# Kernel optimization log

Measured on AMD Instinct MI355X. Metric: run time of the kernel, lower is better.

Reference implementation:

```python
import jax, jax.numpy as jnp
import numpy as np

NUM_CLUSTERS = 512
TEMPERATURE = 1.0
MAX_ITERS = 10
EPSILON = 1e-4
N, D = 65536, 256


def setup_inputs() -> dict:
    key = jax.random.key(0)
    weights = jax.random.normal(key, (N, D), dtype=jnp.float32)
    return {"weights": weights}


def _neg_dist(w, c):
    # -||w_i - c_j||_2 computed via the expanded quadratic form to avoid
    # materializing the [N, K, D] broadcast tensor the torch code builds.
    d2 = (jnp.sum(w * w, axis=1, keepdims=True)
          - 2.0 * (w @ c.T)
          + jnp.sum(c * c, axis=1)[None, :])
    return -jnp.sqrt(jnp.maximum(d2, 1e-12))  # [N, K]


def reference(weights):
    # deterministic stand-in for torch.randperm init: first K rows
    clusters0 = weights[:NUM_CLUSTERS]                                 # [K, D]
    attn0 = jnp.zeros((weights.shape[0], NUM_CLUSTERS), weights.dtype)  # [N, K]
    done0 = jnp.array(False)

    def step(carry, _):
        clusters, attn, done = carry
        attn_new = jax.nn.softmax(_neg_dist(weights, clusters) / TEMPERATURE, axis=-1)
        weighted_sum = attn_new.T @ weights            # [K, D]
        counts = attn_new.sum(axis=0)                  # [K]
        new_clusters = weighted_sum / counts[:, None]
        small = jnp.linalg.norm(clusters - new_clusters) <= EPSILON
        # torch loop: attn is computed BEFORE the break check, clusters only
        # advance if not converged; once done everything is frozen.
        attn_out = jnp.where(done, attn, attn_new)
        clusters_out = jnp.where(done | small, clusters, new_clusters)
        return (clusters_out, attn_out, done | small), None

    (clusters, attn, _), _ = jax.lax.scan(step, (clusters0, attn0, done0), None, length=MAX_ITERS)
    compressed_weights = attn @ clusters               # [N, D]
    return compressed_weights, clusters, attn
```

## Files before the change

kernel.cpp:

```cpp
#include <hip/hip_runtime.h>
#include <math.h>

#define NPTS  65536
#define DIM   256
#define NC    512
#define NITER 10

#define WS_C      0
#define WS_WSUM   (WS_C + NC*DIM)
#define WS_COUNTS (WS_WSUM + NC*DIM)
#define WS_W2     (WS_COUNTS + NC)
#define WS_C2     (WS_W2 + NPTS)
#define WS_DONE   (WS_C2 + NC)
#define WS_CHI    (WS_DONE + 4)
#define WS_CLO    (WS_CHI + NC*DIM/2)

typedef __attribute__((ext_vector_type(8))) short bf16x8;
typedef __attribute__((ext_vector_type(4))) float f32x4;

__device__ __forceinline__ unsigned short f2bf(float x) {
  unsigned u = __float_as_uint(x);
  u += 0x7fffu + ((u >> 16) & 1u);
  return (unsigned short)(u >> 16);
}
__device__ __forceinline__ float bf2f(unsigned short h) {
  return __uint_as_float(((unsigned)h) << 16);
}

__global__ void k_init(const float* __restrict__ W, float* __restrict__ C, int* __restrict__ done) {
  int i = blockIdx.x * 256 + threadIdx.x;
  C[i] = W[i];
  if (i == 0) *done = 0;
}

__global__ void k_w2(const float* __restrict__ W, float* __restrict__ w2) {
  int row  = blockIdx.x * 4 + (threadIdx.x >> 6);
  int lane = threadIdx.x & 63;
  float4 v = *(const float4*)(W + (size_t)row * DIM + 4 * lane);
  float s = v.x*v.x + v.y*v.y + v.z*v.z + v.w*v.w;
  #pragma unroll
  for (int o = 32; o; o >>= 1) s += __shfl_down(s, o);
  if (lane == 0) w2[row] = s;
}

__global__ void k_prep(const float* __restrict__ C, float* __restrict__ c2,
                       float* __restrict__ wsum, float* __restrict__ counts,
                       unsigned short* __restrict__ Chi, unsigned short* __restrict__ Clo) {
  __shared__ float wsh[4];
  int b = blockIdx.x, t = threadIdx.x;
  float v = C[b * DIM + t];
  unsigned short h = f2bf(v);
  Chi[b * DIM + t] = h;
  Clo[b * DIM + t] = f2bf(v - bf2f(h));
  float s = v * v;
  #pragma unroll
  for (int o = 32; o; o >>= 1) s += __shfl_down(s, o);
  if ((t & 63) == 0) wsh[t >> 6] = s;
  __syncthreads();
  if (t == 0) c2[b] = wsh[0] + wsh[1] + wsh[2] + wsh[3];
  wsum[b * DIM + t] = 0.f;
  if (t == 0) counts[b] = 0.f;
}

__launch_bounds__(256, 4)
__global__ void k_attn(const float* __restrict__ W,
                       const unsigned short* __restrict__ Chi,
                       const unsigned short* __restrict__ Clo,
                       const float* __restrict__ w2, const float* __restrict__ c2,
                       float* __restrict__ attn, float* __restrict__ counts,
                       const int* __restrict__ done)
{
  if (*done) return;
  __shared__ unsigned short Bh[2][4096];
  __shared__ unsigned short Bl[2][4096];
  __shared__ float c2s[NC];
  __shared__ float rinv_sh[64];
  __shared__ float cnt_lds[NC];

  const int t    = threadIdx.x;
  const int wave = t >> 6;
  const int lane = t & 63;
  const int lx   = lane & 15;
  const int gy   = lane >> 4;
  const int rowW = blockIdx.x * 64 + wave * 16;

  cnt_lds[t] = 0.f; cnt_lds[t + 256] = 0.f;
  c2s[t] = c2[t];   c2s[t + 256] = c2[t + 256];

  bf16x8 ah[8], al[8];
  {
    const float* wrow = W + (size_t)(rowW + lx) * DIM;
    #pragma unroll
    for (int kc = 0; kc < 8; ++kc) {
      const float* p = wrow + kc * 32 + gy * 8;
      float4 v0 = *(const float4*)p;
      float4 v1 = *(const float4*)(p + 4);
      float xs[8] = {v0.x, v0.y, v0.z, v0.w, v1.x, v1.y, v1.z, v1.w};
      #pragma unroll
      for (int j = 0; j < 8; ++j) {
        unsigned short h = f2bf(xs[j]);
        ah[kc][j] = (short)h;
        al[kc][j] = (short)f2bf(xs[j] - bf2f(h));
      }
    }
  }
  float w2r[4];
  #pragma unroll
  for (int r = 0; r < 4; ++r) w2r[r] = w2[rowW + gy * 4 + r];

  float rowP[4] = {0.f, 0.f, 0.f, 0.f};
  float4 sh[2], sl[2];

  #define STAGE_LOAD(ct_)                                              \
    { _Pragma("unroll")                                                \
      for (int p = 0; p < 2; ++p) {                                    \
        int L = p * 256 + t;                                           \
        int kc = L >> 6, r = (L >> 2) & 15, g = L & 3;                 \
        int off = ((ct_) * 16 + r) * 256 + kc * 32 + g * 8;            \
        sh[p] = *(const float4*)(Chi + off);                           \
        sl[p] = *(const float4*)(Clo + off);                           \
      } }
  #define STAGE_WRITE(b_)                                              \
    { _Pragma("unroll")                                                \
      for (int p = 0; p < 2; ++p) {                                    \
        int L = p * 256 + t;                                           \
        *(float4*)&Bh[b_][L * 8] = sh[p];                              \
        *(float4*)&Bl[b_][L * 8] = sl[p];                              \
      } }

  STAGE_LOAD(0)
  STAGE_WRITE(0)
  __syncthreads();

  for (int ct = 0; ct < 32; ++ct) {
    const int cur = ct & 1;
    if (ct < 31) STAGE_LOAD(ct + 1)

    f32x4 aHH = {0.f,0.f,0.f,0.f}, aLH = {0.f,0.f,0.f,0.f}, aHL = {0.f,0.f,0.f,0.f};
    #pragma unroll
    for (int kc = 0; kc < 8; ++kc) {
      bf16x8 bh = *(const bf16x8*)&Bh[cur][kc * 512 + lx * 32 + gy * 8];
      bf16x8 bl = *(const bf16x8*)&Bl[cur][kc * 512 + lx * 32 + gy * 8];
      aHH = __builtin_amdgcn_mfma_f32_16x16x32_bf16(ah[kc], bh, aHH, 0, 0, 0);
      aLH = __builtin_amdgcn_mfma_f32_16x16x32_bf16(al[kc], bh, aLH, 0, 0, 0);
      aHL = __builtin_amdgcn_mfma_f32_16x16x32_bf16(ah[kc], bl, aHL, 0, 0, 0);
    }
    float c2v = c2s[ct * 16 + lx];
    #pragma unroll
    for (int r = 0; r < 4; ++r) {
      float dot = aHH[r] + aLH[r] + aHL[r];
      float d2  = w2r[r] + c2v - 2.f * dot;
      float e   = __expf(-sqrtf(fmaxf(d2, 1e-12f)));
      rowP[r] += e;
      attn[(size_t)(rowW + gy * 4 + r) * NC + ct * 16 + lx] = e;
    }
    __syncthreads();
    if (ct < 31) { STAGE_WRITE(cur ^ 1) __syncthreads(); }
  }

  #pragma unroll
  for (int m = 1; m < 16; m <<= 1) {
    #pragma unroll
    for (int r = 0; r < 4; ++r) rowP[r] += __shfl_xor(rowP[r], m);
  }
  if (lx == 0) {
    #pragma unroll
    for (int r = 0; r < 4; ++r) rinv_sh[wave * 16 + gy * 4 + r] = 1.f / rowP[r];
  }
  __syncthreads();

  {
    float cs0 = 0.f, cs1 = 0.f, cs2 = 0.f, cs3 = 0.f;
    const int c0 = (t * 4) & 511;
    const size_t base = (size_t)blockIdx.x * 64 * NC;
    #pragma unroll 4
    for (int p = 0; p < 32; ++p) {
      int idx = p * 1024 + t * 4;
      int row = idx >> 9;
      float rv = rinv_sh[row];
      float* g = attn + base + (size_t)row * NC + c0;
      float4 v = *(float4*)g;
      v.x *= rv; v.y *= rv; v.z *= rv; v.w *= rv;
      *(float4*)g = v;
      cs0 += v.x; cs1 += v.y; cs2 += v.z; cs3 += v.w;
    }
    atomicAdd(&cnt_lds[c0 + 0], cs0);
    atomicAdd(&cnt_lds[c0 + 1], cs1);
    atomicAdd(&cnt_lds[c0 + 2], cs2);
    atomicAdd(&cnt_lds[c0 + 3], cs3);
  }
  __syncthreads();
  atomicAdd(&counts[t],       cnt_lds[t]);
  atomicAdd(&counts[t + 256], cnt_lds[t + 256]);
}

__launch_bounds__(256, 2)
__global__ void k_wsum(const float* __restrict__ attn, const float* __restrict__ W,
                       float* __restrict__ wsum, const int* __restrict__ done)
{
  if (*done) return;
  __shared__ float At[64*64];
  __shared__ float Bt[64*64];
  const int t = threadIdx.x, tx = t & 15, ty = t >> 4;
  const int ctile = blockIdx.x & 7;
  const int dtile = (blockIdx.x >> 3) & 3;
  const int kch   = blockIdx.x >> 5;
  const int c0 = ctile*64, d0 = dtile*64;
  const size_t rbase = (size_t)kch * 2048;
  float acc[4][4] = {{0}};
  for (int kk = 0; kk < 2048; kk += 64) {
    __syncthreads();
    #pragma unroll
    for (int p = 0; p < 4; ++p) {
      int q = p*256 + t;
      int kr = q >> 4, c4 = q & 15;
      size_t row = rbase + kk + kr;
      *(float4*)&At[kr*64 + 4*c4] = *(const float4*)(attn + row*NC  + c0 + 4*c4);
      *(float4*)&Bt[kr*64 + 4*c4] = *(const float4*)(W    + row*DIM + d0 + 4*c4);
    }
    __syncthreads();
    #pragma unroll 8
    for (int k = 0; k < 64; ++k) {
      float4 av = *(const float4*)&At[k*64 + 4*ty];
      float4 bv = *(const float4*)&Bt[k*64 + 4*tx];
      acc[0][0]+=av.x*bv.x; acc[0][1]+=av.x*bv.y; acc[0][2]+=av.x*bv.z; acc[0][3]+=av.x*bv.w;
      acc[1][0]+=av.y*bv.x; acc[1][1]+=av.y*bv.y; acc[1][2]+=av.y*bv.z; acc[1][3]+=av.y*bv.w;
      acc[2][0]+=av.z*bv.x; acc[2][1]+=av.z*bv.y; acc[2][2]+=av.z*bv.z; acc[2][3]+=av.z*bv.w;
      acc[3][0]+=av.w*bv.x; acc[3][1]+=av.w*bv.y; acc[3][2]+=av.w*bv.z; acc[3][3]+=av.w*bv.w;
    }
  }
  #pragma unroll
  for (int i = 0; i < 4; ++i)
    #pragma unroll
    for (int j = 0; j < 4; ++j)
      atomicAdd(&wsum[(size_t)(c0 + 4*ty + i)*DIM + d0 + 4*tx + j], acc[i][j]);
}

__global__ void k_update(float* __restrict__ C, const float* __restrict__ wsum,
                         const float* __restrict__ counts, int* __restrict__ done)
{
  if (*done) return;
  __shared__ float wsh[16];
  __shared__ float nrm2;
  int t = threadIdx.x;
  float local = 0.f;
  for (int p = 0; p < 128; ++p) {
    int i = p*1024 + t;
    float cn = wsum[i] / counts[i >> 8];
    float d  = C[i] - cn;
    local += d * d;
  }
  #pragma unroll
  for (int o = 32; o; o >>= 1) local += __shfl_down(local, o);
  if ((t & 63) == 0) wsh[t >> 6] = local;
  __syncthreads();
  if (t == 0) {
    float s = 0.f;
    #pragma unroll
    for (int x = 0; x < 16; ++x) s += wsh[x];
    nrm2 = s;
  }
  __syncthreads();
  if (nrm2 <= 1e-8f) {
    if (t == 0) *done = 1;
  } else {
    for (int p = 0; p < 128; ++p) {
      int i = p*1024 + t;
      C[i] = wsum[i] / counts[i >> 8];
    }
  }
}

__device__ __forceinline__ int swz64(int k, int c) {
  return (k << 6) + (c ^ (((k >> 2) & 15) << 2));
}
__launch_bounds__(256, 2)
__global__ void k_compress(const float* __restrict__ attn, const float* __restrict__ C,
                           float* __restrict__ out)
{
  __shared__ float At[64*64];
  __shared__ float Bt[64*64];
  const int t = threadIdx.x, tx = t & 15, ty = t >> 4;
  const int rt = blockIdx.x >> 2;
  const int dt = blockIdx.x & 3;
  const int r0 = rt*64, d0 = dt*64;
  float acc[4][4] = {{0}};
  for (int kc = 0; kc < 8; ++kc) {
    __syncthreads();
    #pragma unroll
    for (int p = 0; p < 4; ++p) {
      int q = p*256 + t;
      int r = q >> 4, x4 = q & 15;
      float4 v = *(const float4*)(attn + (size_t)(r0 + r)*NC + kc*64 + 4*x4);
      At[swz64(4*x4+0, r)] = v.x;
      At[swz64(4*x4+1, r)] = v.y;
      At[swz64(4*x4+2, r)] = v.z;
      At[swz64(4*x4+3, r)] = v.w;
      *(float4*)&Bt[r*64 + 4*x4] = *(const float4*)(C + (size_t)(kc*64 + r)*DIM + d0 + 4*x4);
    }
    __syncthreads();
    #pragma unroll 8
    for (int k = 0; k < 64; ++k) {
      float4 av = *(const float4*)&At[swz64(k, 4*ty)];
      float4 bv = *(const float4*)&Bt[k*64 + 4*tx];
      acc[0][0]+=av.x*bv.x; acc[0][1]+=av.x*bv.y; acc[0][2]+=av.x*bv.z; acc[0][3]+=av.x*bv.w;
      acc[1][0]+=av.y*bv.x; acc[1][1]+=av.y*bv.y; acc[1][2]+=av.y*bv.z; acc[1][3]+=av.y*bv.w;
      acc[2][0]+=av.z*bv.x; acc[2][1]+=av.z*bv.y; acc[2][2]+=av.z*bv.z; acc[2][3]+=av.z*bv.w;
      acc[3][0]+=av.w*bv.x; acc[3][1]+=av.w*bv.y; acc[3][2]+=av.w*bv.z; acc[3][3]+=av.w*bv.w;
    }
  }
  #pragma unroll
  for (int i = 0; i < 4; ++i) {
    float4 o = {acc[i][0], acc[i][1], acc[i][2], acc[i][3]};
    *(float4*)(out + (size_t)(r0 + 4*ty + i)*DIM + d0 + 4*tx) = o;
  }
}

__global__ void k_copy(const float* __restrict__ C, float* __restrict__ out) {
  int i = blockIdx.x * 256 + threadIdx.x;
  out[i] = C[i];
}

extern "C" void kernel_launch(void* const* d_in, const int* in_sizes, int n_in,
                              void* d_out, int out_size, void* d_ws, size_t ws_size,
                              hipStream_t stream)
{
  const float* W = (const float*)d_in[0];
  float* out = (float*)d_out;
  float* compressed   = out;
  float* out_clusters = out + (size_t)NPTS * DIM;
  float* attn         = out_clusters + NC * DIM;

  float* ws     = (float*)d_ws;
  float* C      = ws + WS_C;
  float* wsum   = ws + WS_WSUM;
  float* counts = ws + WS_COUNTS;
  float* w2     = ws + WS_W2;
  float* c2     = ws + WS_C2;
  int*   done   = (int*)(ws + WS_DONE);
  unsigned short* Chi = (unsigned short*)(ws + WS_CHI);
  unsigned short* Clo = (unsigned short*)(ws + WS_CLO);

  k_init<<<NC*DIM/256, 256, 0, stream>>>(W, C, done);
  k_w2<<<NPTS/4, 256, 0, stream>>>(W, w2);
  for (int it = 0; it < NITER; ++it) {
    k_prep<<<NC, 256, 0, stream>>>(C, c2, wsum, counts, Chi, Clo);
    k_attn<<<NPTS/64, 256, 0, stream>>>(W, Chi, Clo, w2, c2, attn, counts, done);
    k_wsum<<<1024, 256, 0, stream>>>(attn, W, wsum, done);
    k_update<<<1, 1024, 0, stream>>>(C, wsum, counts, done);
  }
  k_compress<<<(NPTS/64)*(DIM/64), 256, 0, stream>>>(attn, C, compressed);
  k_copy<<<NC*DIM/256, 256, 0, stream>>>(C, out_clusters);
}
```

Before: 4.360 ms.

## Defer softmax normalization into wsum and parallelize the cluster update

k_attn now writes unnormalized exponentials and stores per-row reciprocal sums in a global buffer. This removes the per-iteration read-modify-write pass over the 128MB attention matrix. k_wsum scales attention rows by rinv as it loads them and accumulates the cluster counts itself, and a single k_norm pass normalizes attn once at the end. Attention stores are staged through LDS so they go out as coalesced float4 writes, and the B tile becomes single-buffered. The single-block k_update is split into two grid-wide kernels, with the norm reduced through an atomic. The cost is extra kernel launches and more complex convergence bookkeeping.

```diff
diff --git a/kernel.cpp b/kernel.cpp
--- a/kernel.cpp
+++ b/kernel.cpp
@@ -8,11 +8,14 @@
 
 #define WS_C      0
 #define WS_WSUM   (WS_C + NC*DIM)
-#define WS_COUNTS (WS_WSUM + NC*DIM)
+#define WS_CNEW   (WS_WSUM + NC*DIM)
+#define WS_COUNTS (WS_CNEW + NC*DIM)
 #define WS_W2     (WS_COUNTS + NC)
 #define WS_C2     (WS_W2 + NPTS)
-#define WS_DONE   (WS_C2 + NC)
-#define WS_CHI    (WS_DONE + 4)
+#define WS_RINV   (WS_C2 + NC)
+#define WS_DONE   (WS_RINV + NPTS)
+#define WS_NRM    (WS_DONE + 1)
+#define WS_CHI    (WS_DONE + 7)
 #define WS_CLO    (WS_CHI + NC*DIM/2)
 
 typedef __attribute__((ext_vector_type(8))) short bf16x8;
@@ -45,7 +48,8 @@
 
 __global__ void k_prep(const float* __restrict__ C, float* __restrict__ c2,
                        float* __restrict__ wsum, float* __restrict__ counts,
-                       unsigned short* __restrict__ Chi, unsigned short* __restrict__ Clo) {
+                       unsigned short* __restrict__ Chi, unsigned short* __restrict__ Clo,
+                       float* __restrict__ nrm2) {
   __shared__ float wsh[4];
   int b = blockIdx.x, t = threadIdx.x;
   float v = C[b * DIM + t];
@@ -60,6 +64,7 @@
   if (t == 0) c2[b] = wsh[0] + wsh[1] + wsh[2] + wsh[3];
   wsum[b * DIM + t] = 0.f;
   if (t == 0) counts[b] = 0.f;
+  if (b == 0 && t == 0) *nrm2 = 0.f;
 }
 
 __launch_bounds__(256, 4)
@@ -67,15 +72,14 @@
                        const unsigned short* __restrict__ Chi,
                        const unsigned short* __restrict__ Clo,
                        const float* __restrict__ w2, const float* __restrict__ c2,
-                       float* __restrict__ attn, float* __restrict__ counts,
+                       float* __restrict__ attn, float* __restrict__ rinv,
                        const int* __restrict__ done)
 {
   if (*done) return;
-  __shared__ unsigned short Bh[2][4096];
-  __shared__ unsigned short Bl[2][4096];
+  __shared__ unsigned short Bh[4096];
+  __shared__ unsigned short Bl[4096];
   __shared__ float c2s[NC];
-  __shared__ float rinv_sh[64];
-  __shared__ float cnt_lds[NC];
+  __shared__ float ebuf[4][16][36];
 
   const int t    = threadIdx.x;
   const int wave = t >> 6;
@@ -84,8 +88,7 @@
   const int gy   = lane >> 4;
   const int rowW = blockIdx.x * 64 + wave * 16;
 
-  cnt_lds[t] = 0.f; cnt_lds[t + 256] = 0.f;
-  c2s[t] = c2[t];   c2s[t + 256] = c2[t + 256];
+  c2s[t] = c2[t];  c2s[t + 256] = c2[t + 256];
 
   bf16x8 ah[8], al[8];
   {
@@ -111,36 +114,38 @@
   float rowP[4] = {0.f, 0.f, 0.f, 0.f};
   float4 sh[2], sl[2];
 
-  #define STAGE_LOAD(ct_)                                              \
-    { _Pragma("unroll")                                                \
-      for (int p = 0; p < 2; ++p) {                                    \
-        int L = p * 256 + t;                                           \
-        int kc = L >> 6, r = (L >> 2) & 15, g = L & 3;                 \
-        int off = ((ct_) * 16 + r) * 256 + kc * 32 + g * 8;            \
-        sh[p] = *(const float4*)(Chi + off);                           \
-        sl[p] = *(const float4*)(Clo + off);                           \
-      } }
-  #define STAGE_WRITE(b_)                                              \
-    { _Pragma("unroll")                                                \
-      for (int p = 0; p < 2; ++p) {                                    \
-        int L = p * 256 + t;                                           \
-        *(float4*)&Bh[b_][L * 8] = sh[p];                              \
-        *(float4*)&Bl[b_][L * 8] = sl[p];                              \
-      } }
-
-  STAGE_LOAD(0)
-  STAGE_WRITE(0)
+  #pragma unroll
+  for (int p = 0; p < 2; ++p) {
+    int L = p * 256 + t;
+    int kc = L >> 6, r = (L >> 2) & 15, g = L & 3;
+    int off = r * 256 + kc * 32 + g * 8;
+    sh[p] = *(const float4*)(Chi + off);
+    sl[p] = *(const float4*)(Clo + off);
+  }
+  #pragma unroll
+  for (int p = 0; p < 2; ++p) {
+    int L = p * 256 + t;
+    *(float4*)&Bh[L * 8] = sh[p];
+    *(float4*)&Bl[L * 8] = sl[p];
+  }
   __syncthreads();
 
   for (int ct = 0; ct < 32; ++ct) {
-    const int cur = ct & 1;
-    if (ct < 31) STAGE_LOAD(ct + 1)
-
+    if (ct < 31) {
+      #pragma unroll
+      for (int p = 0; p < 2; ++p) {
+        int L = p * 256 + t;
+        int kc = L >> 6, r = (L >> 2) & 15, g = L & 3;
+        int off = ((ct + 1) * 16 + r) * 256 + kc * 32 + g * 8;
+        sh[p] = *(const float4*)(Chi + off);
+        sl[p] = *(const float4*)(Clo + off);
+      }
+    }
     f32x4 aHH = {0.f,0.f,0.f,0.f}, aLH = {0.f,0.f,0.f,0.f}, aHL = {0.f,0.f,0.f,0.f};
     #pragma unroll
     for (int kc = 0; kc < 8; ++kc) {
-      bf16x8 bh = *(const bf16x8*)&Bh[cur][kc * 512 + lx * 32 + gy * 8];
-      bf16x8 bl = *(const bf16x8*)&Bl[cur][kc * 512 + lx * 32 + gy * 8];
+      bf16x8 bh = *(const bf16x8*)&Bh[kc * 512 + lx * 32 + gy * 8];
+      bf16x8 bl = *(const bf16x8*)&Bl[kc * 512 + lx * 32 + gy * 8];
       aHH = __builtin_amdgcn_mfma_f32_16x16x32_bf16(ah[kc], bh, aHH, 0, 0, 0);
       aLH = __builtin_amdgcn_mfma_f32_16x16x32_bf16(al[kc], bh, aLH, 0, 0, 0);
       aHL = __builtin_amdgcn_mfma_f32_16x16x32_bf16(ah[kc], bl, aHL, 0, 0, 0);
@@ -152,10 +157,27 @@
       float d2  = w2r[r] + c2v - 2.f * dot;
       float e   = __expf(-sqrtf(fmaxf(d2, 1e-12f)));
       rowP[r] += e;
-      attn[(size_t)(rowW + gy * 4 + r) * NC + ct * 16 + lx] = e;
-    }
-    __syncthreads();
-    if (ct < 31) { STAGE_WRITE(cur ^ 1) __syncthreads(); }
+      ebuf[wave][gy * 4 + r][(ct & 1) * 16 + lx] = e;
+    }
+    if (ct & 1) {
+      #pragma unroll
+      for (int q = 0; q < 2; ++q) {
+        int r = q * 8 + (lane >> 3);
+        int c = (lane & 7) * 4;
+        float4 v = *(const float4*)&ebuf[wave][r][c];
+        *(float4*)(attn + (size_t)(rowW + r) * NC + (ct & ~1) * 16 + c) = v;
+      }
+    }
+    __syncthreads();
+    if (ct < 31) {
+      #pragma unroll
+      for (int p = 0; p < 2; ++p) {
+        int L = p * 256 + t;
+        *(float4*)&Bh[L * 8] = sh[p];
+        *(float4*)&Bl[L * 8] = sl[p];
+      }
+      __syncthreads();
+    }
   }
 
   #pragma unroll
@@ -165,48 +187,29 @@
   }
   if (lx == 0) {
     #pragma unroll
-    for (int r = 0; r < 4; ++r) rinv_sh[wave * 16 + gy * 4 + r] = 1.f / rowP[r];
-  }
-  __syncthreads();
-
-  {
-    float cs0 = 0.f, cs1 = 0.f, cs2 = 0.f, cs3 = 0.f;
-    const int c0 = (t * 4) & 511;
-    const size_t base = (size_t)blockIdx.x * 64 * NC;
-    #pragma unroll 4
-    for (int p = 0; p < 32; ++p) {
-      int idx = p * 1024 + t * 4;
-      int row = idx >> 9;
-      float rv = rinv_sh[row];
-      float* g = attn + base + (size_t)row * NC + c0;
-      float4 v = *(float4*)g;
-      v.x *= rv; v.y *= rv; v.z *= rv; v.w *= rv;
-      *(float4*)g = v;
-      cs0 += v.x; cs1 += v.y; cs2 += v.z; cs3 += v.w;
-    }
-    atomicAdd(&cnt_lds[c0 + 0], cs0);
-    atomicAdd(&cnt_lds[c0 + 1], cs1);
-    atomicAdd(&cnt_lds[c0 + 2], cs2);
-    atomicAdd(&cnt_lds[c0 + 3], cs3);
-  }
-  __syncthreads();
-  atomicAdd(&counts[t],       cnt_lds[t]);
-  atomicAdd(&counts[t + 256], cnt_lds[t + 256]);
+    for (int r = 0; r < 4; ++r) rinv[rowW + gy * 4 + r] = 1.f / rowP[r];
+  }
 }
 
 __launch_bounds__(256, 2)
 __global__ void k_wsum(const float* __restrict__ attn, const float* __restrict__ W,
-                       float* __restrict__ wsum, const int* __restrict__ done)
+                       const float* __restrict__ rinv,
+                       float* __restrict__ wsum, float* __restrict__ counts,
+                       const int* __restrict__ done)
 {
   if (*done) return;
   __shared__ float At[64*64];
   __shared__ float Bt[64*64];
+  __shared__ float cnt_sh[64];
   const int t = threadIdx.x, tx = t & 15, ty = t >> 4;
   const int ctile = blockIdx.x & 7;
   const int dtile = (blockIdx.x >> 3) & 3;
   const int kch   = blockIdx.x >> 5;
   const int c0 = ctile*64, d0 = dtile*64;
   const size_t rbase = (size_t)kch * 2048;
+  const bool do_cnt = (dtile == 0);
+  if (t < 64) cnt_sh[t] = 0.f;
+  float cs0 = 0.f, cs1 = 0.f, cs2 = 0.f, cs3 = 0.f;
   float acc[4][4] = {{0}};
   for (int kk = 0; kk < 2048; kk += 64) {
     __syncthreads();
@@ -215,8 +218,12 @@
       int q = p*256 + t;
       int kr = q >> 4, c4 = q & 15;
       size_t row = rbase + kk + kr;
-      *(float4*)&At[kr*64 + 4*c4] = *(const float4*)(attn + row*NC  + c0 + 4*c4);
-      *(float4*)&Bt[kr*64 + 4*c4] = *(const float4*)(W    + row*DIM + d0 + 4*c4);
+      float4 a = *(const float4*)(attn + row*NC + c0 + 4*c4);
+      float rv = rinv[row];
+      a.x *= rv; a.y *= rv; a.z *= rv; a.w *= rv;
+      if (do_cnt) { cs0 += a.x; cs1 += a.y; cs2 += a.z; cs3 += a.w; }
+      *(float4*)&At[kr*64 + 4*c4] = a;
+      *(float4*)&Bt[kr*64 + 4*c4] = *(const float4*)(W + row*DIM + d0 + 4*c4);
     }
     __syncthreads();
     #pragma unroll 8
@@ -234,41 +241,51 @@
     #pragma unroll
     for (int j = 0; j < 4; ++j)
       atomicAdd(&wsum[(size_t)(c0 + 4*ty + i)*DIM + d0 + 4*tx + j], acc[i][j]);
-}
-
-__global__ void k_update(float* __restrict__ C, const float* __restrict__ wsum,
-                         const float* __restrict__ counts, int* __restrict__ done)
+  if (do_cnt) {
+    atomicAdd(&cnt_sh[4*tx + 0], cs0);
+    atomicAdd(&cnt_sh[4*tx + 1], cs1);
+    atomicAdd(&cnt_sh[4*tx + 2], cs2);
+    atomicAdd(&cnt_sh[4*tx + 3], cs3);
+    __syncthreads();
+    if (t < 64) atomicAdd(&counts[c0 + t], cnt_sh[t]);
+  }
+}
+
+__global__ void k_updA(const float* __restrict__ C, const float* __restrict__ wsum,
+                       const float* __restrict__ counts, float* __restrict__ Cnew,
+                       float* __restrict__ nrm2, const int* __restrict__ done)
 {
   if (*done) return;
-  __shared__ float wsh[16];
-  __shared__ float nrm2;
-  int t = threadIdx.x;
-  float local = 0.f;
-  for (int p = 0; p < 128; ++p) {
-    int i = p*1024 + t;
-    float cn = wsum[i] / counts[i >> 8];
-    float d  = C[i] - cn;
-    local += d * d;
-  }
-  #pragma unroll
-  for (int o = 32; o; o >>= 1) local += __shfl_down(local, o);
-  if ((t & 63) == 0) wsh[t >> 6] = local;
+  __shared__ float sh[4];
+  int i = blockIdx.x * 256 + threadIdx.x;
+  float cn = wsum[i] / counts[i >> 8];
+  Cnew[i] = cn;
+  float d = C[i] - cn;
+  float s = d * d;
+  #pragma unroll
+  for (int o = 32; o; o >>= 1) s += __shfl_down(s, o);
+  if ((threadIdx.x & 63) == 0) sh[threadIdx.x >> 6] = s;
   __syncthreads();
-  if (t == 0) {
-    float s = 0.f;
-    #pragma unroll
-    for (int x = 0; x < 16; ++x) s += wsh[x];
-    nrm2 = s;
-  }
-  __syncthreads();
-  if (nrm2 <= 1e-8f) {
-    if (t == 0) *done = 1;
+  if (threadIdx.x == 0) atomicAdd(nrm2, sh[0] + sh[1] + sh[2] + sh[3]);
+}
+__global__ void k_updB(float* __restrict__ C, const float* __restrict__ Cnew,
+                       const float* __restrict__ nrm2, int* __restrict__ done)
+{
+  if (*done) return;
+  if (*nrm2 <= 1e-8f) {
+    if (blockIdx.x == 0 && threadIdx.x == 0) *done = 1;
   } else {
-    for (int p = 0; p < 128; ++p) {
-      int i = p*1024 + t;
-      C[i] = wsum[i] / counts[i >> 8];
-    }
-  }
+    int i = blockIdx.x * 256 + threadIdx.x;
+    C[i] = Cnew[i];
+  }
+}
+
+__global__ void k_norm(float* __restrict__ attn, const float* __restrict__ rinv) {
+  size_t i = ((size_t)blockIdx.x * 256 + threadIdx.x) * 4;
+  float rv = rinv[i >> 9];
+  float4 v = *(float4*)(attn + i);
+  v.x *= rv; v.y *= rv; v.z *= rv; v.w *= rv;
+  *(float4*)(attn + i) = v;
 }
 
 __device__ __forceinline__ int swz64(int k, int c) {
@@ -334,21 +351,26 @@
   float* ws     = (float*)d_ws;
   float* C      = ws + WS_C;
   float* wsum   = ws + WS_WSUM;
+  float* Cnew   = ws + WS_CNEW;
   float* counts = ws + WS_COUNTS;
   float* w2     = ws + WS_W2;
   float* c2     = ws + WS_C2;
+  float* rinv   = ws + WS_RINV;
   int*   done   = (int*)(ws + WS_DONE);
+  float* nrm2   = ws + WS_NRM;
   unsigned short* Chi = (unsigned short*)(ws + WS_CHI);
   unsigned short* Clo = (unsigned short*)(ws + WS_CLO);
 
   k_init<<<NC*DIM/256, 256, 0, stream>>>(W, C, done);
   k_w2<<<NPTS/4, 256, 0, stream>>>(W, w2);
   for (int it = 0; it < NITER; ++it) {
-    k_prep<<<NC, 256, 0, stream>>>(C, c2, wsum, counts, Chi, Clo);
-    k_attn<<<NPTS/64, 256, 0, stream>>>(W, Chi, Clo, w2, c2, attn, counts, done);
-    k_wsum<<<1024, 256, 0, stream>>>(attn, W, wsum, done);
-    k_update<<<1, 1024, 0, stream>>>(C, wsum, counts, done);
-  }
+    k_prep<<<NC, 256, 0, stream>>>(C, c2, wsum, counts, Chi, Clo, nrm2);
+    k_attn<<<NPTS/64, 256, 0, stream>>>(W, Chi, Clo, w2, c2, attn, rinv, done);
+    k_wsum<<<1024, 256, 0, stream>>>(attn, W, rinv, wsum, counts, done);
+    k_updA<<<NC*DIM/256, 256, 0, stream>>>(C, wsum, counts, Cnew, nrm2, done);
+    k_updB<<<NC*DIM/256, 256, 0, stream>>>(C, Cnew, nrm2, done);
+  }
+  k_norm<<<NPTS*NC/1024, 256, 0, stream>>>(attn, rinv);
   k_compress<<<(NPTS/64)*(DIM/64), 256, 0, stream>>>(attn, C, compressed);
   k_copy<<<NC*DIM/256, 256, 0, stream>>>(C, out_clusters);
 }
```

After: 3.731 ms. -14.4%, faster.
